# Optimization experiments

Measured on AMD Instinct MI355X. Metric: run time of the kernel, lower is better.

The kernel has to match this reference:

```python
import jax, jax.numpy as jnp
import numpy as np

SIGMA = 1e-4   # SoftRas coverage sharpness
GAMMA = 0.1    # depth-softmax temperature
IMAGE_SIZE = 128


def _normalize(v):
    return v / (jnp.linalg.norm(v, axis=-1, keepdims=True) + 1e-8)


def _look_at(eye, center, up):
    z = _normalize(eye - center)
    x = _normalize(jnp.cross(up, z))
    y = jnp.cross(z, x)
    R = jnp.stack([x, y, z], axis=-2)                       # (B,3,3)
    t = -jnp.einsum('bij,bj->bi', R, eye)
    B = eye.shape[0]
    M = jnp.tile(jnp.eye(4, dtype=eye.dtype), (B, 1, 1))
    M = M.at[:, :3, :3].set(R).at[:, :3, 3].set(t)
    return M


def _perspective(fov_y, aspect, near, far):
    f = 1.0 / np.tan(fov_y / 2.0)
    M = np.zeros((4, 4), np.float32)
    M[0, 0] = f / aspect
    M[1, 1] = f
    M[2, 2] = (far + near) / (near - far)
    M[2, 3] = 2.0 * far * near / (near - far)
    M[3, 2] = -1.0
    return jnp.asarray(M)


def _project(verts_world, eye, center, up):
    B, V, _ = verts_world.shape
    view = _look_at(eye, center, up)
    proj = _perspective(np.deg2rad(60.0), 1.0, 0.1, 10.0)
    M = jnp.einsum('ij,bjk->bik', proj, view)
    vh = jnp.concatenate([verts_world, jnp.ones((B, V, 1), verts_world.dtype)], -1)
    clip = jnp.einsum('bij,bvj->bvi', M, vh)
    return clip[..., :3] / (clip[..., 3:4] + 1e-8)            # (B,V,3) NDC


def _edge_dist(p, a, b):
    # p: (H,W,2); a,b: (B,F,2) -> unsigned point-to-segment distance (B,F,H,W)
    pa = p[None, None] - a[:, :, None, None]                  # (B,F,H,W,2)
    ba = (b - a)[:, :, None, None]                            # (B,F,1,1,2)
    t = jnp.clip(jnp.sum(pa * ba, -1) / (jnp.sum(ba * ba, -1) + 1e-12), 0.0, 1.0)
    d = pa - t[..., None] * ba
    return jnp.sqrt(jnp.sum(d * d, -1) + 1e-12)


def _cross2(u, v):
    return u[..., 0] * v[..., 1] - u[..., 1] * v[..., 0]


def _rasterize(verts_ndc, faces, colors, image_size):
    tri = verts_ndc[:, faces]                                 # (B,F,3,3)
    v2, vz = tri[..., :2], tri[..., 2]                        # (B,F,3,2), (B,F,3)
    xs = (jnp.arange(image_size) + 0.5) / image_size * 2.0 - 1.0
    ys = 1.0 - (jnp.arange(image_size) + 0.5) / image_size * 2.0
    X, Y = jnp.meshgrid(xs, ys, indexing='xy')
    p = jnp.stack([X, Y], -1)                                 # (H,W,2)

    a0, a1, a2 = v2[:, :, 0], v2[:, :, 1], v2[:, :, 2]        # (B,F,2)
    area = _cross2(a1 - a0, a2 - a0)[:, :, None, None]        # (B,F,1,1)
    denom = area + jnp.where(area >= 0, 1e-12, -1e-12)
    w0 = _cross2((a2 - a1)[:, :, None, None], p[None, None] - a1[:, :, None, None])
    w1 = _cross2((a0 - a2)[:, :, None, None], p[None, None] - a2[:, :, None, None])
    w2 = _cross2((a1 - a0)[:, :, None, None], p[None, None] - a0[:, :, None, None])
    b0, b1, b2 = w0 / denom, w1 / denom, w2 / denom           # barycentrics (B,F,H,W)
    inside = (b0 >= 0) & (b1 >= 0) & (b2 >= 0)

    d = jnp.minimum(jnp.minimum(_edge_dist(p, a0, a1), _edge_dist(p, a1, a2)),
                    _edge_dist(p, a2, a0))
    sgn = jnp.where(inside, 1.0, -1.0)
    prob = jax.nn.sigmoid(sgn * d * d / SIGMA)                # soft coverage (B,F,H,W)
    sil = 1.0 - jnp.prod(1.0 - prob, axis=1, keepdims=True)   # (B,1,H,W)

    bc0, bc1, bc2 = (jnp.clip(b0, 0., 1.), jnp.clip(b1, 0., 1.), jnp.clip(b2, 0., 1.))
    s = bc0 + bc1 + bc2 + 1e-8
    zpix = (bc0 * vz[:, :, 0, None, None] + bc1 * vz[:, :, 1, None, None]
            + bc2 * vz[:, :, 2, None, None]) / s
    zn = jnp.clip((1.0 - zpix) * 0.5, 0.0, 1.0)               # 1 = near
    m = jnp.max(zn, axis=1, keepdims=True)
    Dw = prob * jnp.exp((zn - m) / GAMMA)
    w_bg = jnp.exp((0.0 - m) / GAMMA)                         # background (far, black)
    Wn = Dw / (jnp.sum(Dw, axis=1, keepdims=True) + w_bg)     # (B,F,H,W)
    face_col = jnp.mean(colors[:, faces], axis=2)             # (B,F,3)
    rgb = jnp.einsum('bfhw,bfc->bchw', Wn, face_col)          # (B,3,H,W)
    return sil, rgb


def setup_inputs() -> dict:
    key = jax.random.key(0)
    k1, k2, k3, k4 = jax.random.split(key, 4)
    B, V, F = 4, 256, 256
    verts_world = jax.random.normal(k1, (B, V, 3), jnp.float32) * 0.5
    faces = jax.random.randint(k2, (F, 3), 0, V)
    colors = jax.random.uniform(k3, (B, V, 3), jnp.float32)
    eye = jnp.tile(jnp.array([0.0, 0.0, 2.5], jnp.float32), (B, 1)) \
          + jax.random.normal(k4, (B, 3), jnp.float32) * 0.05
    return {"verts_world": verts_world, "faces": faces, "colors": colors, "eye": eye}


def reference(verts_world, faces, colors, eye):
    B = verts_world.shape[0]
    center = jnp.zeros((B, 3), verts_world.dtype)
    up = jnp.tile(jnp.array([0.0, 1.0, 0.0], verts_world.dtype), (B, 1))
    verts_ndc = _project(verts_world, eye, center, up)
    return _rasterize(verts_ndc, faces, colors, IMAGE_SIZE)
```

## Files before the change

### kernel.cpp

```cpp
#include <hip/hip_runtime.h>

#define NB 4
#define NV 256
#define NF 256
#define IMG 128
#define STR 32

typedef float v2f __attribute__((ext_vector_type(2)));

__device__ __forceinline__ float rcpf(float x) { return __builtin_amdgcn_rcpf(x); }
__device__ __forceinline__ float ex2(float x)  { return __builtin_amdgcn_exp2f(x); }
__device__ __forceinline__ float med01(float x) { return __builtin_amdgcn_fmed3f(x, 0.0f, 1.0f); }
__device__ __forceinline__ v2f med01_2(v2f v) { return (v2f){ med01(v.x), med01(v.y) }; }
__device__ __forceinline__ v2f fma2(v2f a, v2f b, v2f c) { return __builtin_elementwise_fma(a, b, c); }


__global__ void prep_faces(const float* __restrict__ verts,
                           const int* __restrict__ faces,
                           const float* __restrict__ colors,
                           const float* __restrict__ eye,
                           float* __restrict__ fd)
{
    int gid = blockIdx.x * blockDim.x + threadIdx.x;
    if (gid >= NB * NF) return;
    int b = gid >> 8;
    int f = gid & 255;

    const float fpj = 1.7320508075688772f;
    const float p22 = -1.0202020202020203f;
    const float p23 = -0.20202020202020202f;
    const float SC   = 120.11224139682566f;
    const float ISC2 = 6.931471805599453e-05f;

    float ex = eye[b*3+0], ey = eye[b*3+1], ez = eye[b*3+2];
    float en  = sqrtf(ex*ex + ey*ey + ez*ez);
    float izn = 1.0f / (en + 1e-8f);
    float zx = ex*izn, zy = ey*izn, zz = ez*izn;
    float cn  = sqrtf(zz*zz + zx*zx);
    float ixn = 1.0f / (cn + 1e-8f);
    float xx = zz*ixn, xy = 0.0f, xz = -zx*ixn;
    float yx = zy*xz - zz*xy;
    float yy = zz*xx - zx*xz;
    float yz = zx*xy - zy*xx;
    float tx = -(xx*ex + xy*ey + xz*ez);
    float ty = -(yx*ex + yy*ey + yz*ez);
    float tz = -(zx*ex + zy*ey + zz*ez);

    int i0 = faces[f*3+0], i1 = faces[f*3+1], i2 = faces[f*3+2];
    int idx[3] = { i0, i1, i2 };

    float ax[3], ay[3], az[3];
#pragma unroll
    for (int k = 0; k < 3; ++k) {
        const float* v = verts + (b*NV + idx[k])*3;
        float vx = v[0], vy = v[1], vz = v[2];
        float cx  = fpj*(xx*vx + xy*vy + xz*vz + tx);
        float cyv = fpj*(yx*vx + yy*vy + yz*vz + ty);
        float zv  = zx*vx + zy*vy + zz*vz + tz;
        float cz  = p22*zv + p23;
        float cw  = -zv;
        float iw  = 1.0f / (cw + 1e-8f);
        ax[k] = cx*iw; ay[k] = cyv*iw; az[k] = cz*iw;
    }

    float a0x = ax[0], a0y = ay[0];
    float a1x = ax[1], a1y = ay[1];
    float a2x = ax[2], a2y = ay[2];

    float e01x = a1x - a0x, e01y = a1y - a0y;
    float e12x = a2x - a1x, e12y = a2y - a1y;
    float e20x = a0x - a2x, e20y = a0y - a2y;

    float area  = e01x*(a2y - a0y) - e01y*(a2x - a0x);
    float denom = area + (area >= 0.0f ? 1e-12f : -1e-12f);
    float idn   = 1.0f / denom;

    float ib01 = 1.0f / (e01x*e01x + e01y*e01y + 1e-12f);
    float ib12 = 1.0f / (e12x*e12x + e12y*e12y + 1e-12f);
    float ib20 = 1.0f / (e20x*e20x + e20y*e20y + 1e-12f);

    const float third = (1.0f/3.0f);
    float cr = (colors[(b*NV+i0)*3+0] + colors[(b*NV+i1)*3+0] + colors[(b*NV+i2)*3+0]) * third;
    float cg = (colors[(b*NV+i0)*3+1] + colors[(b*NV+i1)*3+1] + colors[(b*NV+i2)*3+1]) * third;
    float cb = (colors[(b*NV+i0)*3+2] + colors[(b*NV+i1)*3+2] + colors[(b*NV+i2)*3+2]) * third;

    float* o = fd + (b*128 + (f >> 1))*STR + (f & 1);
    o[ 0]=a0x*SC;   o[ 2]=a0y*SC;
    o[ 4]=e01x*SC;  o[ 6]=e01y*SC;
    o[ 8]=e12x*SC;  o[10]=e12y*SC;
    o[12]=ib01*ISC2; o[14]=ib12*ISC2; o[16]=ib20*ISC2;
    o[18]=idn*ISC2;
    o[20]=az[0]; o[22]=az[1]; o[24]=az[2];
    o[26]=cr;   o[28]=cg;   o[30]=cb;
}

__launch_bounds__(512, 4)
__global__ void raster(const float* __restrict__ fd, float* __restrict__ out)
{
    __shared__ float sFD[5120];

    const int t   = threadIdx.x;
    const int cy  = threadIdx.y;
    const int b   = blockIdx.x >> 7;
    const int grp = blockIdx.x & 127;
    const int pix0 = grp*128 + t;
    const int pix1 = pix0 + 64;

    {
        const float4* src = (const float4*)(fd + (b << 12));
        float4* dst = (float4*)sFD;
        int tid = (cy << 6) + t;
        dst[tid]       = src[tid];
        dst[tid + 512] = src[tid + 512];
    }
    __syncthreads();

    const float SC = 120.11224139682566f;
    const float KGAM = 14.426950408889634f;
    const v2f KGH_NEG = { -0.5f*KGAM, -0.5f*KGAM };
    const v2f KGH_POS = {  0.5f*KGAM,  0.5f*KGAM };
    const v2f ONE2 = { 1.0f, 1.0f };
    const v2f EPS2 = { 1e-8f, 1e-8f };

    const int h0 = pix0 >> 7, w0 = pix0 & 127;
    const int h1 = pix1 >> 7, w1 = pix1 & 127;
    const float pxa = ((w0 + 0.5f) * (1.0f/64.0f) - 1.0f) * SC;
    const float pya = (1.0f - (h0 + 0.5f) * (1.0f/64.0f)) * SC;
    const float pxb = ((w1 + 0.5f) * (1.0f/64.0f) - 1.0f) * SC;
    const float pyb = (1.0f - (h1 + 0.5f) * (1.0f/64.0f)) * SC;
    const v2f PXA = { pxa, pxa }, PYA = { pya, pya };
    const v2f PXB = { pxb, pxb }, PYB = { pyb, pyb };

    const float* fc = sFD + cy*(16*STR);

    v2f A_prod = ONE2, A_S = {0,0}, A_R0 = {0,0}, A_R1 = {0,0}, A_R2 = {0,0};
    v2f B_prod = ONE2, B_S = {0,0}, B_R0 = {0,0}, B_R1 = {0,0}, B_R2 = {0,0};

#define PIXEL(PXS, PYS, AP, AS, AR0, AR1, AR2) do {                      \
    v2f pa0x = PXS - a0x, pa0y = PYS - a0y;                              \
    v2f pa1x = pa0x - e01x, pa1y = pa0y - e01y;                          \
    v2f pa2x = pa0x + e20x, pa2y = pa0y + e20y;                          \
    v2f b0 = fma2(-e12y, pa1x, e12x*pa1y) * idn;                         \
    v2f b1 = fma2(-e20y, pa2x, e20x*pa2y) * idn;                         \
    v2f b2 = fma2(-e01y, pa0x, e01x*pa0y) * idn;                         \
    v2f tt = med01_2(fma2(pa0x, g01x, pa0y*g01y));                       \
    v2f dx = fma2(-tt, e01x, pa0x);                                      \
    v2f dy = fma2(-tt, e01y, pa0y);                                      \
    v2f dd0 = fma2(dx, dx, dy*dy);                                       \
    tt = med01_2(fma2(pa1x, g12x, pa1y*g12y));                           \
    dx = fma2(-tt, e12x, pa1x);                                          \
    dy = fma2(-tt, e12y, pa1y);                                          \
    v2f dd1 = fma2(dx, dx, dy*dy);                                       \
    tt = med01_2(fma2(pa2x, g20x, pa2y*g20y));                           \
    dx = fma2(-tt, e20x, pa2x);                                          \
    dy = fma2(-tt, e20y, pa2y);                                          \
    v2f dd2 = fma2(dx, dx, dy*dy);                                       \
    float ddl = fminf(fminf(dd0.x, dd1.x), dd2.x);                       \
    float ddh = fminf(fminf(dd0.y, dd1.y), dd2.y);                       \
    float mxl = fmaxf(fmaxf(-b0.x, -b1.x), -b2.x);                       \
    float mxh = fmaxf(fmaxf(-b0.y, -b1.y), -b2.y);                       \
    float qx = copysignf(ddl, mxl);                                      \
    float qy = copysignf(ddh, mxh);                                      \
    v2f e2 = { ex2(qx), ex2(qy) };                                       \
    v2f den = e2 + ONE2;                                                 \
    v2f prob = { rcpf(den.x), rcpf(den.y) };                             \
    AP = fma2(-prob, AP, AP);                                            \
    v2f bc0 = med01_2(b0), bc1 = med01_2(b1), bc2 = med01_2(b2);         \
    v2f s = (bc0 + bc1) + (bc2 + EPS2);                                  \
    v2f zs = fma2(bc0, z0, fma2(bc1, z1, bc2*z2));                       \
    v2f irs = { rcpf(s.x), rcpf(s.y) };                                  \
    v2f zq = fma2(zs*irs, KGH_NEG, KGH_POS);                             \
    float znx = __builtin_amdgcn_fmed3f(zq.x, 0.0f, KGAM);               \
    float zny = __builtin_amdgcn_fmed3f(zq.y, 0.0f, KGAM);               \
    v2f ez = { ex2(znx), ex2(zny) };                                     \
    v2f wgt = prob * ez;                                                 \
    AS = AS + wgt;                                                       \
    AR0 = fma2(wgt, cr, AR0);                                            \
    AR1 = fma2(wgt, cg, AR1);                                            \
    AR2 = fma2(wgt, cb, AR2);                                            \
} while (0)

    for (int i = 0; i < 16; ++i) {
        const float* c = fc + i*STR;
#define LD(k) (*(const v2f*)(c + 2*(k)))
        v2f a0x = LD(0), a0y = LD(1);
        v2f e01x = LD(2), e01y = LD(3);
        v2f e12x = LD(4), e12y = LD(5);
        v2f ib01 = LD(6), ib12 = LD(7), ib20 = LD(8);
        v2f idn = LD(9);
        v2f z0 = LD(10), z1 = LD(11), z2 = LD(12);
        v2f cr = LD(13), cg = LD(14), cb = LD(15);
#undef LD
        v2f e20x = -(e01x + e12x), e20y = -(e01y + e12y);
        v2f g01x = e01x*ib01, g01y = e01y*ib01;
        v2f g12x = e12x*ib12, g12y = e12y*ib12;
        v2f g20x = e20x*ib20, g20y = e20y*ib20;

        PIXEL(PXA, PYA, A_prod, A_S, A_R0, A_R1, A_R2);
        PIXEL(PXB, PYB, B_prod, B_S, B_R0, B_R1, B_R2);
    }
#undef PIXEL

    __syncthreads();
    float* red = sFD;
    red[((0*2+0)*8 + cy)*64 + t] = A_prod.x * A_prod.y;
    red[((0*2+1)*8 + cy)*64 + t] = B_prod.x * B_prod.y;
    red[((1*2+0)*8 + cy)*64 + t] = A_S.x  + A_S.y;
    red[((1*2+1)*8 + cy)*64 + t] = B_S.x  + B_S.y;
    red[((2*2+0)*8 + cy)*64 + t] = A_R0.x + A_R0.y;
    red[((2*2+1)*8 + cy)*64 + t] = B_R0.x + B_R0.y;
    red[((3*2+0)*8 + cy)*64 + t] = A_R1.x + A_R1.y;
    red[((3*2+1)*8 + cy)*64 + t] = B_R1.x + B_R1.y;
    red[((4*2+0)*8 + cy)*64 + t] = A_R2.x + A_R2.y;
    red[((4*2+1)*8 + cy)*64 + t] = B_R2.x + B_R2.y;
    __syncthreads();

    if (cy == 0) {
#pragma unroll
        for (int j = 0; j < 2; ++j) {
            float P  = 1.0f, St = 0.0f, r0 = 0.0f, r1 = 0.0f, r2 = 0.0f;
#pragma unroll
            for (int c2 = 0; c2 < 8; ++c2) {
                P  *= red[((0*2+j)*8 + c2)*64 + t];
                St += red[((1*2+j)*8 + c2)*64 + t];
                r0 += red[((2*2+j)*8 + c2)*64 + t];
                r1 += red[((3*2+j)*8 + c2)*64 + t];
                r2 += red[((4*2+j)*8 + c2)*64 + t];
            }
            float iden = rcpf(St + 1.0f);
            int pix = (j == 0) ? pix0 : pix1;

            out[b*16384 + pix] = 1.0f - P;
            float* rgb = out + 65536;
            rgb[(b*3 + 0)*16384 + pix] = r0 * iden;
            rgb[(b*3 + 1)*16384 + pix] = r1 * iden;
            rgb[(b*3 + 2)*16384 + pix] = r2 * iden;
        }
    }
}

extern "C" void kernel_launch(void* const* d_in, const int* in_sizes, int n_in,
                              void* d_out, int out_size, void* d_ws, size_t ws_size,
                              hipStream_t stream)
{
    const float* verts  = (const float*)d_in[0];
    const int*   faces  = (const int*)d_in[1];
    const float* colors = (const float*)d_in[2];
    const float* eye    = (const float*)d_in[3];
    float* out = (float*)d_out;
    float* fd  = (float*)d_ws;

    hipLaunchKernelGGL(prep_faces, dim3(4), dim3(256), 0, stream,
                       verts, faces, colors, eye, fd);
    hipLaunchKernelGGL(raster, dim3(512), dim3(64, 8), 0, stream, fd, out);
}
```

Measured before the change: 33.27 us.

## Tile pixels into 16x16 blocks and skip far faces per wavefront

Result: faster. 31.24 us (-6.1%).

```diff
diff --git a/kernel.cpp b/kernel.cpp
--- a/kernel.cpp
+++ b/kernel.cpp
@@ -94,24 +94,24 @@
     o[26]=cr;   o[28]=cg;   o[30]=cb;
 }
 
-__launch_bounds__(512, 4)
+__launch_bounds__(1024)
 __global__ void raster(const float* __restrict__ fd, float* __restrict__ out)
 {
-    __shared__ float sFD[5120];
-
-    const int t   = threadIdx.x;
-    const int cy  = threadIdx.y;
-    const int b   = blockIdx.x >> 7;
-    const int grp = blockIdx.x & 127;
-    const int pix0 = grp*128 + t;
-    const int pix1 = pix0 + 64;
+    __shared__ float sMEM[20480];
+
+    const int t    = threadIdx.x;
+    const int cy   = threadIdx.y;
+    const int bId  = blockIdx.x;
+    const int b    = bId >> 6;
+    const int tile = bId & 63;
+    const int tX = (tile & 7) << 4;
+    const int tY = (tile >> 3) << 4;
+    const int lx = t & 7, ly = t >> 3;
 
     {
         const float4* src = (const float4*)(fd + (b << 12));
-        float4* dst = (float4*)sFD;
-        int tid = (cy << 6) + t;
-        dst[tid]       = src[tid];
-        dst[tid + 512] = src[tid + 512];
+        float4* dst = (float4*)sMEM;
+        dst[cy*64 + t] = src[cy*64 + t];
     }
     __syncthreads();
 
@@ -122,65 +122,69 @@
     const v2f ONE2 = { 1.0f, 1.0f };
     const v2f EPS2 = { 1e-8f, 1e-8f };
 
-    const int h0 = pix0 >> 7, w0 = pix0 & 127;
-    const int h1 = pix1 >> 7, w1 = pix1 & 127;
-    const float pxa = ((w0 + 0.5f) * (1.0f/64.0f) - 1.0f) * SC;
-    const float pya = (1.0f - (h0 + 0.5f) * (1.0f/64.0f)) * SC;
-    const float pxb = ((w1 + 0.5f) * (1.0f/64.0f) - 1.0f) * SC;
-    const float pyb = (1.0f - (h1 + 0.5f) * (1.0f/64.0f)) * SC;
-    const v2f PXA = { pxa, pxa }, PYA = { pya, pya };
-    const v2f PXB = { pxb, pxb }, PYB = { pyb, pyb };
-
-    const float* fc = sFD + cy*(16*STR);
-
-    v2f A_prod = ONE2, A_S = {0,0}, A_R0 = {0,0}, A_R1 = {0,0}, A_R2 = {0,0};
-    v2f B_prod = ONE2, B_S = {0,0}, B_R0 = {0,0}, B_R1 = {0,0}, B_R2 = {0,0};
-
-#define PIXEL(PXS, PYS, AP, AS, AR0, AR1, AR2) do {                      \
-    v2f pa0x = PXS - a0x, pa0y = PYS - a0y;                              \
-    v2f pa1x = pa0x - e01x, pa1y = pa0y - e01y;                          \
-    v2f pa2x = pa0x + e20x, pa2y = pa0y + e20y;                          \
-    v2f b0 = fma2(-e12y, pa1x, e12x*pa1y) * idn;                         \
-    v2f b1 = fma2(-e20y, pa2x, e20x*pa2y) * idn;                         \
-    v2f b2 = fma2(-e01y, pa0x, e01x*pa0y) * idn;                         \
-    v2f tt = med01_2(fma2(pa0x, g01x, pa0y*g01y));                       \
-    v2f dx = fma2(-tt, e01x, pa0x);                                      \
-    v2f dy = fma2(-tt, e01y, pa0y);                                      \
-    v2f dd0 = fma2(dx, dx, dy*dy);                                       \
-    tt = med01_2(fma2(pa1x, g12x, pa1y*g12y));                           \
-    dx = fma2(-tt, e12x, pa1x);                                          \
-    dy = fma2(-tt, e12y, pa1y);                                          \
-    v2f dd1 = fma2(dx, dx, dy*dy);                                       \
-    tt = med01_2(fma2(pa2x, g20x, pa2y*g20y));                           \
-    dx = fma2(-tt, e20x, pa2x);                                          \
-    dy = fma2(-tt, e20y, pa2y);                                          \
-    v2f dd2 = fma2(dx, dx, dy*dy);                                       \
-    float ddl = fminf(fminf(dd0.x, dd1.x), dd2.x);                       \
-    float ddh = fminf(fminf(dd0.y, dd1.y), dd2.y);                       \
-    float mxl = fmaxf(fmaxf(-b0.x, -b1.x), -b2.x);                       \
-    float mxh = fmaxf(fmaxf(-b0.y, -b1.y), -b2.y);                       \
-    float qx = copysignf(ddl, mxl);                                      \
-    float qy = copysignf(ddh, mxh);                                      \
-    v2f e2 = { ex2(qx), ex2(qy) };                                       \
-    v2f den = e2 + ONE2;                                                 \
-    v2f prob = { rcpf(den.x), rcpf(den.y) };                             \
-    AP = fma2(-prob, AP, AP);                                            \
-    v2f bc0 = med01_2(b0), bc1 = med01_2(b1), bc2 = med01_2(b2);         \
-    v2f s = (bc0 + bc1) + (bc2 + EPS2);                                  \
-    v2f zs = fma2(bc0, z0, fma2(bc1, z1, bc2*z2));                       \
-    v2f irs = { rcpf(s.x), rcpf(s.y) };                                  \
-    v2f zq = fma2(zs*irs, KGH_NEG, KGH_POS);                             \
-    float znx = __builtin_amdgcn_fmed3f(zq.x, 0.0f, KGAM);               \
-    float zny = __builtin_amdgcn_fmed3f(zq.y, 0.0f, KGAM);               \
-    v2f ez = { ex2(znx), ex2(zny) };                                     \
-    v2f wgt = prob * ez;                                                 \
-    AS = AS + wgt;                                                       \
-    AR0 = fma2(wgt, cr, AR0);                                            \
-    AR1 = fma2(wgt, cg, AR1);                                            \
-    AR2 = fma2(wgt, cb, AR2);                                            \
-} while (0)
-
-    for (int i = 0; i < 16; ++i) {
+    const float x0 = ((tX + lx + 0.5f) * (1.0f/64.0f) - 1.0f) * SC;
+    const float x1 = ((tX + lx + 8.5f) * (1.0f/64.0f) - 1.0f) * SC;
+    const float y0 = (1.0f - (tY + ly + 0.5f) * (1.0f/64.0f)) * SC;
+    const float y1 = (1.0f - (tY + ly + 8.5f) * (1.0f/64.0f)) * SC;
+    const v2f PX0 = { x0, x0 }, PX1 = { x1, x1 };
+    const v2f PY0 = { y0, y0 }, PY1 = { y1, y1 };
+
+    const float* fc = sMEM + cy*(8*STR);
+
+    v2f aP0 = ONE2, aS0 = {0,0}, aR00 = {0,0}, aR10 = {0,0}, aR20 = {0,0};
+    v2f aP1 = ONE2, aS1 = {0,0}, aR01 = {0,0}, aR11 = {0,0}, aR21 = {0,0};
+    v2f aP2 = ONE2, aS2 = {0,0}, aR02 = {0,0}, aR12 = {0,0}, aR22 = {0,0};
+    v2f aP3 = ONE2, aS3 = {0,0}, aR03 = {0,0}, aR13 = {0,0}, aR23 = {0,0};
+
+#define PH1(J, PXS, PYS)                                                  \
+    v2f pa0x##J = PXS - a0x, pa0y##J = PYS - a0y;                         \
+    v2f pa1x##J = pa0x##J - e01x, pa1y##J = pa0y##J - e01y;               \
+    v2f pa2x##J = pa0x##J + e20x, pa2y##J = pa0y##J + e20y;               \
+    v2f b0##J = fma2(-e12y, pa1x##J, e12x*pa1y##J) * idn;                 \
+    v2f b1##J = fma2(-e20y, pa2x##J, e20x*pa2y##J) * idn;                 \
+    v2f b2##J = fma2(-e01y, pa0x##J, e01x*pa0y##J) * idn;                 \
+    v2f q##J;                                                             \
+    {                                                                     \
+        v2f tt = med01_2(fma2(pa0x##J, g01x, pa0y##J*g01y));              \
+        v2f dx = fma2(-tt, e01x, pa0x##J);                                \
+        v2f dy = fma2(-tt, e01y, pa0y##J);                                \
+        v2f ddA = fma2(dx, dx, dy*dy);                                    \
+        tt = med01_2(fma2(pa1x##J, g12x, pa1y##J*g12y));                  \
+        dx = fma2(-tt, e12x, pa1x##J);                                    \
+        dy = fma2(-tt, e12y, pa1y##J);                                    \
+        v2f ddB = fma2(dx, dx, dy*dy);                                    \
+        tt = med01_2(fma2(pa2x##J, g20x, pa2y##J*g20y));                  \
+        dx = fma2(-tt, e20x, pa2x##J);                                    \
+        dy = fma2(-tt, e20y, pa2y##J);                                    \
+        v2f ddC = fma2(dx, dx, dy*dy);                                    \
+        float ddl = fminf(fminf(ddA.x, ddB.x), ddC.x);                    \
+        float ddh = fminf(fminf(ddA.y, ddB.y), ddC.y);                    \
+        float mxl = fmaxf(fmaxf(-b0##J.x, -b1##J.x), -b2##J.x);           \
+        float mxh = fmaxf(fmaxf(-b0##J.y, -b1##J.y), -b2##J.y);           \
+        q##J = (v2f){ copysignf(ddl, mxl), copysignf(ddh, mxh) };         \
+    }
+
+#define PH2(J, AP, AS, AR0, AR1, AR2)                                     \
+    {                                                                     \
+        v2f e2 = { ex2(q##J.x), ex2(q##J.y) };                            \
+        v2f den = e2 + ONE2;                                              \
+        v2f prob = { rcpf(den.x), rcpf(den.y) };                          \
+        AP = fma2(-prob, AP, AP);                                         \
+        v2f bc0 = med01_2(b0##J), bc1 = med01_2(b1##J), bc2 = med01_2(b2##J); \
+        v2f s = (bc0 + bc1) + (bc2 + EPS2);                               \
+        v2f zs = fma2(bc0, z0, fma2(bc1, z1, bc2*z2));                    \
+        v2f irs = { rcpf(s.x), rcpf(s.y) };                               \
+        v2f zq = fma2(zs*irs, KGH_NEG, KGH_POS);                          \
+        v2f ez = { ex2(__builtin_amdgcn_fmed3f(zq.x, 0.0f, KGAM)),        \
+                   ex2(__builtin_amdgcn_fmed3f(zq.y, 0.0f, KGAM)) };      \
+        v2f wgt = prob * ez;                                              \
+        AS = AS + wgt;                                                    \
+        AR0 = fma2(wgt, cr, AR0);                                         \
+        AR1 = fma2(wgt, cg, AR1);                                         \
+        AR2 = fma2(wgt, cb, AR2);                                         \
+    }
+
+    for (int i = 0; i < 8; ++i) {
         const float* c = fc + i*STR;
 #define LD(k) (*(const v2f*)(c + 2*(k)))
         v2f a0x = LD(0), a0y = LD(1);
@@ -196,46 +200,56 @@
         v2f g12x = e12x*ib12, g12y = e12y*ib12;
         v2f g20x = e20x*ib20, g20y = e20y*ib20;
 
-        PIXEL(PXA, PYA, A_prod, A_S, A_R0, A_R1, A_R2);
-        PIXEL(PXB, PYB, B_prod, B_S, B_R0, B_R1, B_R2);
-    }
-#undef PIXEL
+        PH1(0, PX0, PY0)
+        PH1(1, PX1, PY0)
+        PH1(2, PX0, PY1)
+        PH1(3, PX1, PY1)
+
+        float qm = fminf(fminf(fminf(q0.x, q0.y), fminf(q1.x, q1.y)),
+                         fminf(fminf(q2.x, q2.y), fminf(q3.x, q3.y)));
+        if (!__all(qm > 32.0f)) {
+            PH2(0, aP0, aS0, aR00, aR10, aR20)
+            PH2(1, aP1, aS1, aR01, aR11, aR21)
+            PH2(2, aP2, aS2, aR02, aR12, aR22)
+            PH2(3, aP3, aS3, aR03, aR13, aR23)
+        }
+    }
+#undef PH1
+#undef PH2
 
     __syncthreads();
-    float* red = sFD;
-    red[((0*2+0)*8 + cy)*64 + t] = A_prod.x * A_prod.y;
-    red[((0*2+1)*8 + cy)*64 + t] = B_prod.x * B_prod.y;
-    red[((1*2+0)*8 + cy)*64 + t] = A_S.x  + A_S.y;
-    red[((1*2+1)*8 + cy)*64 + t] = B_S.x  + B_S.y;
-    red[((2*2+0)*8 + cy)*64 + t] = A_R0.x + A_R0.y;
-    red[((2*2+1)*8 + cy)*64 + t] = B_R0.x + B_R0.y;
-    red[((3*2+0)*8 + cy)*64 + t] = A_R1.x + A_R1.y;
-    red[((3*2+1)*8 + cy)*64 + t] = B_R1.x + B_R1.y;
-    red[((4*2+0)*8 + cy)*64 + t] = A_R2.x + A_R2.y;
-    red[((4*2+1)*8 + cy)*64 + t] = B_R2.x + B_R2.y;
+    float* red = sMEM;
+#define ST(A, J, V) red[(((A)*4 + (J))*16 + cy)*64 + t] = (V);
+    ST(0,0, aP0.x*aP0.y)  ST(0,1, aP1.x*aP1.y)  ST(0,2, aP2.x*aP2.y)  ST(0,3, aP3.x*aP3.y)
+    ST(1,0, aS0.x+aS0.y)  ST(1,1, aS1.x+aS1.y)  ST(1,2, aS2.x+aS2.y)  ST(1,3, aS3.x+aS3.y)
+    ST(2,0, aR00.x+aR00.y) ST(2,1, aR01.x+aR01.y) ST(2,2, aR02.x+aR02.y) ST(2,3, aR03.x+aR03.y)
+    ST(3,0, aR10.x+aR10.y) ST(3,1, aR11.x+aR11.y) ST(3,2, aR12.x+aR12.y) ST(3,3, aR13.x+aR13.y)
+    ST(4,0, aR20.x+aR20.y) ST(4,1, aR21.x+aR21.y) ST(4,2, aR22.x+aR22.y) ST(4,3, aR23.x+aR23.y)
+#undef ST
     __syncthreads();
 
-    if (cy == 0) {
+    if (cy < 4) {
+        const int j = cy;
+        const int w = tX + lx + (j & 1)*8;
+        const int h = tY + ly + (j >> 1)*8;
+        const int pix = h*IMG + w;
+
+        float P = 1.0f, St = 0.0f, r0 = 0.0f, r1 = 0.0f, r2 = 0.0f;
 #pragma unroll
-        for (int j = 0; j < 2; ++j) {
-            float P  = 1.0f, St = 0.0f, r0 = 0.0f, r1 = 0.0f, r2 = 0.0f;
-#pragma unroll
-            for (int c2 = 0; c2 < 8; ++c2) {
-                P  *= red[((0*2+j)*8 + c2)*64 + t];
-                St += red[((1*2+j)*8 + c2)*64 + t];
-                r0 += red[((2*2+j)*8 + c2)*64 + t];
-                r1 += red[((3*2+j)*8 + c2)*64 + t];
-                r2 += red[((4*2+j)*8 + c2)*64 + t];
-            }
-            float iden = rcpf(St + 1.0f);
-            int pix = (j == 0) ? pix0 : pix1;
-
-            out[b*16384 + pix] = 1.0f - P;
-            float* rgb = out + 65536;
-            rgb[(b*3 + 0)*16384 + pix] = r0 * iden;
-            rgb[(b*3 + 1)*16384 + pix] = r1 * iden;
-            rgb[(b*3 + 2)*16384 + pix] = r2 * iden;
+        for (int c2 = 0; c2 < 16; ++c2) {
+            P  *= red[((0*4 + j)*16 + c2)*64 + t];
+            St += red[((1*4 + j)*16 + c2)*64 + t];
+            r0 += red[((2*4 + j)*16 + c2)*64 + t];
+            r1 += red[((3*4 + j)*16 + c2)*64 + t];
+            r2 += red[((4*4 + j)*16 + c2)*64 + t];
         }
+        float iden = rcpf(St + 1.0f);
+
+        out[b*16384 + pix] = 1.0f - P;
+        float* rgb = out + 65536;
+        rgb[(b*3 + 0)*16384 + pix] = r0 * iden;
+        rgb[(b*3 + 1)*16384 + pix] = r1 * iden;
+        rgb[(b*3 + 2)*16384 + pix] = r2 * iden;
     }
 }
 
@@ -252,5 +266,5 @@
 
     hipLaunchKernelGGL(prep_faces, dim3(4), dim3(256), 0, stream,
                        verts, faces, colors, eye, fd);
-    hipLaunchKernelGGL(raster, dim3(512), dim3(64, 8), 0, stream, fd, out);
+    hipLaunchKernelGGL(raster, dim3(256), dim3(64, 16), 0, stream, fd, out);
 }
```
